# Performance work log

Measured on AMD Instinct MI355X. Metric: run time of the kernel, lower is better.

Reference implementation:

```python
import jax, jax.numpy as jnp
import numpy as np
from jax import lax

B, S, D, F, E, K = 4, 2048, 2048, 8192, 8, 2


def setup_inputs() -> dict:
    key = jax.random.key(0)
    ks = jax.random.split(key, 4)
    sd = 1.0 / np.sqrt(D)
    sf = 1.0 / np.sqrt(F)
    return {
        "hidden_states": jax.random.normal(ks[0], (B, S, D), dtype=jnp.float32),
        "router_w": jax.random.normal(ks[1], (D, E), dtype=jnp.float32) * sd,
        "w1": jax.random.normal(ks[2], (E, D, F), dtype=jnp.float32) * sd,
        "b1": jnp.zeros((E, F), dtype=jnp.float32),
        "w2": jax.random.normal(ks[3], (E, F, D), dtype=jnp.float32) * sf,
        "b2": jnp.zeros((E, D), dtype=jnp.float32),
        "top_k": K,
    }


def reference(hidden_states, router_w, w1, b1, w2, b2, top_k):
    b, s, d = hidden_states.shape
    x = hidden_states.reshape(-1, d)  # [T, D] flat tokens
    # Router: top-k over expert logits, softmax over the selected logits.
    logits = x @ router_w                      # [T, E]
    top_vals, top_idx = lax.top_k(logits, top_k)  # [T, K]
    scores = jax.nn.softmax(top_vals, axis=-1)    # [T, K]

    out = jnp.zeros_like(x)
    n_experts = w1.shape[0]
    for e in range(n_experts):  # fixed small expert count
        # per-token combine weight for this expert (0 if not routed)
        cw = jnp.sum(jnp.where(top_idx == e, scores, 0.0), axis=-1)  # [T]
        h = jax.nn.gelu(x @ w1[e] + b1[e], approximate=False)        # [T, F]
        out = out + cw[:, None] * (h @ w2[e] + b2[e])                # masked combine
    out = out.reshape(b, s, d)
    return out + hidden_states  # use_residual=True
```

## Files before the change

### kernel.cpp

```cpp
#include <hip/hip_runtime.h>

#define T_TOK 8192
#define DIM   2048
#define FFN   8192
#define NE    8
#define TOPK  2

typedef unsigned short ushort_t;
typedef unsigned short ushort8  __attribute__((ext_vector_type(8)));
typedef unsigned short ushort4v __attribute__((ext_vector_type(4)));
typedef short bf16x8 __attribute__((ext_vector_type(8)));
typedef float f32x4  __attribute__((ext_vector_type(4)));

__device__ __forceinline__ ushort_t f2bf(float f) {
  unsigned int u = __float_as_uint(f);
  u += 0x7FFFu + ((u >> 16) & 1u);
  return (ushort_t)(u >> 16);
}
__device__ __forceinline__ float bf2f(ushort_t u) {
  return __uint_as_float(((unsigned int)u) << 16);
}

__device__ __forceinline__ void gload16(const void* g, void* l) {
  __builtin_amdgcn_global_load_lds((const __attribute__((address_space(1))) void*)g,
                                   (__attribute__((address_space(3))) void*)l, 16, 0, 0);
}
__device__ __forceinline__ unsigned lds_off(const ushort_t* p) {
  return (unsigned)(uintptr_t)(__attribute__((address_space(3))) const ushort_t*)p;
}
__device__ __forceinline__ bf16x8 ds_read128(unsigned off) {
  bf16x8 r;
  asm volatile("ds_read_b128 %0, %1" : "=v"(r) : "v"(off));
  return r;
}

__device__ __forceinline__ float gelu_exact(float v) {
  float s = v * 0.70710678118654752f;
  float a = fabsf(s);
  float t = __builtin_amdgcn_rcpf(1.0f + 0.3275911f * a);
  float p = t * (0.254829592f +
            t * (-0.284496736f +
            t * (1.421413741f +
            t * (-1.453152027f +
            t * 1.061405429f))));
  float er = 1.0f - p * __expf(-a * a);
  er = copysignf(er, s);
  return 0.5f * v * (1.0f + er);
}

__global__ void k_cast(const float* __restrict__ x, ushort_t* __restrict__ xbf) {
  int i = blockIdx.x * blockDim.x + threadIdx.x;
  float4 v = reinterpret_cast<const float4*>(x)[i];
  ushort4v o;
  o.x = f2bf(v.x); o.y = f2bf(v.y); o.z = f2bf(v.z); o.w = f2bf(v.w);
  reinterpret_cast<ushort4v*>(xbf)[i] = o;
}

#define TT 64
__global__ __launch_bounds__(256) void k_wcvt(const float* __restrict__ in,
                                              ushort_t* __restrict__ outp, int R, int C) {
  __shared__ ushort_t t[TT][TT + 8];
  int e = blockIdx.z;
  const float* src = in + (size_t)e * R * C;
  ushort_t* dst = outp + (size_t)e * R * C;
  int r0 = blockIdx.y * TT, c0 = blockIdx.x * TT;
  int tid = threadIdx.x;
  int rr = tid >> 4;
  int c4 = tid & 15;
#pragma unroll
  for (int i = 0; i < 4; i++) {
    int r = rr + i * 16;
    float4 v = *reinterpret_cast<const float4*>(src + (size_t)(r0 + r) * C + c0 + c4 * 4);
    ushort4v p;
    p.x = f2bf(v.x); p.y = f2bf(v.y); p.z = f2bf(v.z); p.w = f2bf(v.w);
    *reinterpret_cast<ushort4v*>(&t[r][c4 * 4]) = p;
  }
  __syncthreads();
  int c = tid >> 2, rs = tid & 3;
  ushort_t tmp[16];
#pragma unroll
  for (int i = 0; i < 16; i++) tmp[i] = t[rs * 16 + i][c];
  ushort8 v0, v1;
#pragma unroll
  for (int i = 0; i < 8; i++) { v0[i] = tmp[i]; v1[i] = tmp[8 + i]; }
  ushort_t* drow = dst + (size_t)(c0 + c) * R + r0 + rs * 16;
  *reinterpret_cast<ushort8*>(drow) = v0;
  *reinterpret_cast<ushort8*>(drow + 8) = v1;
}

__global__ __launch_bounds__(256) void k_router(
    const float* __restrict__ x, const float* __restrict__ rw,
    int* __restrict__ tidx, float* __restrict__ twt, int* __restrict__ counts) {
  int t = blockIdx.x;
  int tid = threadIdx.x;
  int lane = tid & 63, wave = tid >> 6;
  float acc[NE];
#pragma unroll
  for (int e = 0; e < NE; e++) acc[e] = 0.f;
  const float* xr = x + (size_t)t * DIM;
  for (int d = tid; d < DIM; d += 256) {
    float xv = xr[d];
    const float* r = rw + d * NE;
#pragma unroll
    for (int e = 0; e < NE; e++) acc[e] += xv * r[e];
  }
  __shared__ float wsum[4][NE];
#pragma unroll
  for (int e = 0; e < NE; e++) {
    float v = acc[e];
#pragma unroll
    for (int off = 32; off > 0; off >>= 1) v += __shfl_down(v, off);
    if (lane == 0) wsum[wave][e] = v;
  }
  __syncthreads();
  if (tid == 0) {
    float lg[NE];
#pragma unroll
    for (int e = 0; e < NE; e++) lg[e] = wsum[0][e] + wsum[1][e] + wsum[2][e] + wsum[3][e];
    int i0 = 0; float v0 = lg[0];
#pragma unroll
    for (int e = 1; e < NE; e++) if (lg[e] > v0) { v0 = lg[e]; i0 = e; }
    int i1 = -1; float v1 = -3.4e38f;
#pragma unroll
    for (int e = 0; e < NE; e++) if (e != i0 && lg[e] > v1) { v1 = lg[e]; i1 = e; }
    float e1 = expf(v1 - v0);
    float s = 1.f + e1;
    tidx[t * 2 + 0] = i0; tidx[t * 2 + 1] = i1;
    twt[t * 2 + 0] = 1.f / s; twt[t * 2 + 1] = e1 / s;
    atomicAdd(&counts[i0], 1);
    atomicAdd(&counts[i1], 1);
  }
}

__global__ void k_scan(const int* __restrict__ counts, int* __restrict__ offsets) {
  if (threadIdx.x == 0) {
    int s = 0;
    for (int e = 0; e < NE; e++) { offsets[e] = s; s += counts[e]; }
    offsets[NE] = s;
  }
}

__global__ void k_fill(const int* __restrict__ tidx, const float* __restrict__ twt,
                       const int* __restrict__ offsets, int* __restrict__ cursors,
                       int* __restrict__ ltok, float* __restrict__ lwt, int* __restrict__ ppos) {
  int t = blockIdx.x * blockDim.x + threadIdx.x;
  if (t >= T_TOK) return;
#pragma unroll
  for (int k = 0; k < TOPK; k++) {
    int e = tidx[t * 2 + k];
    int pos = atomicAdd(&cursors[e], 1);
    int p = offsets[e] + pos;
    ltok[p] = t;
    lwt[p] = twt[t * 2 + k];
    ppos[t * 2 + k] = p;
  }
}

#define BM 256
#define BN 256
#define BK 32
#define SLOT (BM * BK)
#define SLOTB (SLOT * 2)

__device__ __forceinline__ void xcd_decode(int lin, int nwg, int nx, int& xt, int& yt) {
  int q = nwg >> 3;
  int w = (lin & 7) * q + (lin >> 3);
  xt = w % nx;
  yt = w / nx;
}

template <int NT>
__device__ __forceinline__ void gemm_loop(const ushort_t* __restrict__ a0,
                                          const ushort_t* __restrict__ a1,
                                          const ushort_t* __restrict__ b0,
                                          const ushort_t* __restrict__ b1,
                                          ushort_t* AsLds, ushort_t* BsLds,
                                          f32x4 (&acc)[8][4]) {
  int tid = threadIdx.x;
  int wid = tid >> 6, lane = tid & 63;
  int wm = wid >> 2, wn = wid & 3;
  int lm = lane & 15, lg = lane >> 4;

  unsigned abase = lds_off(AsLds), bbase = lds_off(BsLds);
  unsigned aoff[8], boff[4];
#pragma unroll
  for (int m = 0; m < 8; m++)
    aoff[m] = abase + (unsigned)(((wm * 128 + m * 16 + lm) * BK + lg * 8) * 2);
#pragma unroll
  for (int n = 0; n < 4; n++)
    boff[n] = bbase + (unsigned)(((wn * 64 + n * 16 + lm) * BK + lg * 8) * 2);

  const ushort_t* ap[2] = {a0, a1};
  const ushort_t* bp[2] = {b0, b1};

  auto STAGE = [&](int buf, int k0) {
#pragma unroll
    for (int j = 0; j < 2; j++) {
      gload16(ap[j] + k0, AsLds + buf * SLOT + (j * 512 + wid * 64) * 8);
      gload16(bp[j] + k0, BsLds + buf * SLOT + (j * 512 + wid * 64) * 8);
    }
  };

  STAGE(0, 0);
  STAGE(1, BK);
  int cur = 0;
  for (int t = 0; t < NT; ++t) {
    int s2 = cur + 2; if (s2 >= 3) s2 -= 3;
    if (t + 2 < NT) {
      STAGE(s2, (t + 2) * BK);
      __builtin_amdgcn_sched_barrier(0);
      asm volatile("s_waitcnt vmcnt(8)" ::: "memory");
    } else if (t + 1 < NT) {
      __builtin_amdgcn_sched_barrier(0);
      asm volatile("s_waitcnt vmcnt(4)" ::: "memory");
    } else {
      __builtin_amdgcn_sched_barrier(0);
      asm volatile("s_waitcnt vmcnt(0)" ::: "memory");
    }
    __builtin_amdgcn_s_barrier();
    __builtin_amdgcn_sched_barrier(0);
    unsigned cb = (unsigned)(cur * SLOTB);
    bf16x8 af[8], bv[4];
#pragma unroll
    for (int m = 0; m < 8; m++) af[m] = ds_read128(aoff[m] + cb);
#pragma unroll
    for (int n = 0; n < 4; n++) bv[n] = ds_read128(boff[n] + cb);
    asm volatile("s_waitcnt lgkmcnt(0)" ::: "memory");
    __builtin_amdgcn_sched_barrier(0);
    __builtin_amdgcn_s_setprio(1);
#pragma unroll
    for (int m = 0; m < 8; m++)
#pragma unroll
      for (int n = 0; n < 4; n++)
        acc[m][n] = __builtin_amdgcn_mfma_f32_16x16x32_bf16(af[m], bv[n], acc[m][n], 0, 0, 0);
    __builtin_amdgcn_s_setprio(0);
    __builtin_amdgcn_sched_barrier(0);
    __builtin_amdgcn_s_barrier();
    __builtin_amdgcn_sched_barrier(0);
    cur += 1; if (cur == 3) cur = 0;
  }
}

__global__ __launch_bounds__(512) void k_gemm1(
    const ushort_t* __restrict__ xbf, const ushort_t* __restrict__ w1t, const float* __restrict__ b1,
    const int* __restrict__ counts, const int* __restrict__ offsets,
    const int* __restrict__ ltok, ushort_t* __restrict__ H) {
  int e = blockIdx.z;
  int cnt = counts[e];
  int xt, yt;
  xcd_decode(blockIdx.x, (T_TOK / BM) * (FFN / BN), T_TOK / BM, xt, yt);
  int row0 = xt * BM;
  if (row0 >= cnt) return;
  int base = offsets[e];
  int col0 = yt * BN;
  const ushort_t* Bt = w1t + (size_t)e * DIM * FFN;

  __shared__ __align__(16) ushort_t As[3 * SLOT];
  __shared__ __align__(16) ushort_t Bs[3 * SLOT];

  int tid = threadIdx.x;
  int rsub = tid >> 2, seg = tid & 3;
  const ushort_t* asrc[2]; const ushort_t* bsrc[2];
#pragma unroll
  for (int j = 0; j < 2; j++) {
    int row = j * 128 + rsub;
    int ar = min(row0 + row, cnt - 1);
    asrc[j] = xbf + (size_t)ltok[base + ar] * DIM + seg * 8;
    bsrc[j] = Bt + (size_t)(col0 + row) * DIM + seg * 8;
  }
  f32x4 acc[8][4];
#pragma unroll
  for (int m = 0; m < 8; m++)
#pragma unroll
    for (int n = 0; n < 4; n++) acc[m][n] = (f32x4){0.f, 0.f, 0.f, 0.f};

  gemm_loop<DIM / BK>(asrc[0], asrc[1], bsrc[0], bsrc[1], As, Bs, acc);

  int wid = tid >> 6, lane = tid & 63;
  int wm = wid >> 2, wn = wid & 3;
  int lm = lane & 15, lg = lane >> 4;
#pragma unroll
  for (int m = 0; m < 8; m++) {
#pragma unroll
    for (int n = 0; n < 4; n++) {
      int f = col0 + wn * 64 + n * 16 + lm;
      float bias = b1[e * FFN + f];
#pragma unroll
      for (int r = 0; r < 4; r++) {
        int row = row0 + wm * 128 + m * 16 + lg * 4 + r;
        if (row < cnt) {
          float v = acc[m][n][r] + bias;
          H[(size_t)(base + row) * FFN + f] = f2bf(gelu_exact(v));
        }
      }
    }
  }
}

__global__ __launch_bounds__(512) void k_gemm2(
    const ushort_t* __restrict__ H, const ushort_t* __restrict__ w2t, const float* __restrict__ b2,
    const int* __restrict__ counts, const int* __restrict__ offsets,
    const float* __restrict__ lwt, ushort_t* __restrict__ contrib) {
  int e = blockIdx.z;
  int cnt = counts[e];
  int xt, yt;
  xcd_decode(blockIdx.x, (T_TOK / BM) * (DIM / BN), T_TOK / BM, xt, yt);
  int row0 = xt * BM;
  if (row0 >= cnt) return;
  int base = offsets[e];
  int col0 = yt * BN;
  const ushort_t* Bt = w2t + (size_t)e * DIM * FFN;

  __shared__ __align__(16) ushort_t As[3 * SLOT];
  __shared__ __align__(16) ushort_t Bs[3 * SLOT];

  int tid = threadIdx.x;
  int rsub = tid >> 2, seg = tid & 3;
  const ushort_t* asrc[2]; const ushort_t* bsrc[2];
#pragma unroll
  for (int j = 0; j < 2; j++) {
    int row = j * 128 + rsub;
    int ar = min(row0 + row, cnt - 1);
    asrc[j] = H + (size_t)(base + ar) * FFN + seg * 8;
    bsrc[j] = Bt + (size_t)(col0 + row) * FFN + seg * 8;
  }
  f32x4 acc[8][4];
#pragma unroll
  for (int m = 0; m < 8; m++)
#pragma unroll
    for (int n = 0; n < 4; n++) acc[m][n] = (f32x4){0.f, 0.f, 0.f, 0.f};

  gemm_loop<FFN / BK>(asrc[0], asrc[1], bsrc[0], bsrc[1], As, Bs, acc);

  int wid = tid >> 6, lane = tid & 63;
  int wm = wid >> 2, wn = wid & 3;
  int lm = lane & 15, lg = lane >> 4;
#pragma unroll
  for (int m = 0; m < 8; m++) {
#pragma unroll
    for (int n = 0; n < 4; n++) {
      int d = col0 + wn * 64 + n * 16 + lm;
      float bias = b2[e * DIM + d];
#pragma unroll
      for (int r = 0; r < 4; r++) {
        int row = row0 + wm * 128 + m * 16 + lg * 4 + r;
        if (row < cnt) {
          float v = (acc[m][n][r] + bias) * lwt[base + row];
          contrib[(size_t)(base + row) * DIM + d] = f2bf(v);
        }
      }
    }
  }
}

__global__ void k_combine(const float* __restrict__ x, const ushort_t* __restrict__ contrib,
                          const int* __restrict__ ppos, float* __restrict__ out) {
  int i = blockIdx.x * blockDim.x + threadIdx.x;
  int t = i / (DIM / 4);
  int dq = i % (DIM / 4);
  int p0 = ppos[t * 2 + 0], p1 = ppos[t * 2 + 1];
  float4 xv = reinterpret_cast<const float4*>(x)[i];
  ushort4v c0 = reinterpret_cast<const ushort4v*>(contrib + (size_t)p0 * DIM)[dq];
  ushort4v c1 = reinterpret_cast<const ushort4v*>(contrib + (size_t)p1 * DIM)[dq];
  float4 o;
  o.x = xv.x + bf2f(c0.x) + bf2f(c1.x);
  o.y = xv.y + bf2f(c0.y) + bf2f(c1.y);
  o.z = xv.z + bf2f(c0.z) + bf2f(c1.z);
  o.w = xv.w + bf2f(c0.w) + bf2f(c1.w);
  reinterpret_cast<float4*>(out)[i] = o;
}

extern "C" void kernel_launch(void* const* d_in, const int* in_sizes, int n_in,
                              void* d_out, int out_size, void* d_ws, size_t ws_size,
                              hipStream_t stream) {
  const float* x  = (const float*)d_in[0];
  const float* rw = (const float*)d_in[1];
  const float* w1 = (const float*)d_in[2];
  const float* b1 = (const float*)d_in[3];
  const float* w2 = (const float*)d_in[4];
  const float* b2 = (const float*)d_in[5];
  float* out = (float*)d_out;
  char* ws = (char*)d_ws;

  const size_t MB = 1u << 20;
  int*   counts  = (int*)(ws);
  int*   offsets = (int*)(ws + 64);
  int*   cursors = (int*)(ws + 128);
  int*   tidx    = (int*)(ws + 1 * MB);
  float* twt     = (float*)(ws + 2 * MB);
  int*   ltok    = (int*)(ws + 3 * MB);
  float* lwt     = (float*)(ws + 4 * MB);
  int*   ppos    = (int*)(ws + 5 * MB);
  ushort_t* xbf     = (ushort_t*)(ws + 8 * MB);
  ushort_t* contrib = (ushort_t*)(ws + 8 * MB);
  ushort_t* Hbuf    = (ushort_t*)(ws + 72 * MB);
  ushort_t* w1t     = (ushort_t*)(ws + 328 * MB);
  ushort_t* w2t     = (ushort_t*)(ws + 328 * MB);
  const size_t NEED = 584 * MB;
  if (ws_size < NEED) {
    hipMemsetAsync(d_out, 0, (size_t)out_size * sizeof(float), stream);
    return;
  }

  hipMemsetAsync(ws, 0, 256, stream);
  k_cast<<<dim3((T_TOK * (size_t)DIM / 4) / 256), 256, 0, stream>>>(x, xbf);
  k_router<<<T_TOK, 256, 0, stream>>>(x, rw, tidx, twt, counts);
  k_scan<<<1, 64, 0, stream>>>(counts, offsets);
  k_fill<<<T_TOK / 256, 256, 0, stream>>>(tidx, twt, offsets, cursors, ltok, lwt, ppos);
  k_wcvt<<<dim3(FFN / TT, DIM / TT, NE), 256, 0, stream>>>(w1, w1t, DIM, FFN);
  k_gemm1<<<dim3((T_TOK / BM) * (FFN / BN), 1, NE), 512, 0, stream>>>(xbf, w1t, b1, counts, offsets, ltok, Hbuf);
  k_wcvt<<<dim3(DIM / TT, FFN / TT, NE), 256, 0, stream>>>(w2, w2t, FFN, DIM);
  k_gemm2<<<dim3((T_TOK / BM) * (DIM / BN), 1, NE), 512, 0, stream>>>(Hbuf, w2t, b2, counts, offsets, lwt, contrib);
  k_combine<<<dim3((T_TOK * (size_t)DIM / 4) / 256), 256, 0, stream>>>(x, contrib, ppos, out);
}
```

Before: 2.338 ms.

## XOR-swizzle LDS tiles and interleave A-fragment reads with MFMA groups

Applies an XOR swizzle to the 16-byte chunk position within each LDS row, on both the global-to-LDS staging side and the ds_read side. The aim is to cut LDS bank conflicts on the 128-bit reads. It also splits the per-tile MFMA block into four groups, reading two A fragments per group so LDS reads overlap with the previous group's MFMAs and fewer fragment registers are live. The extra s_barrier inside each group adds workgroup-wide synchronisation that could stall warps.

```diff
diff --git a/kernel.cpp b/kernel.cpp
--- a/kernel.cpp
+++ b/kernel.cpp
@@ -180,15 +180,16 @@
   int wid = tid >> 6, lane = tid & 63;
   int wm = wid >> 2, wn = wid & 3;
   int lm = lane & 15, lg = lane >> 4;
+  int pc = lg ^ (lm & 3);
 
   unsigned abase = lds_off(AsLds), bbase = lds_off(BsLds);
   unsigned aoff[8], boff[4];
 #pragma unroll
   for (int m = 0; m < 8; m++)
-    aoff[m] = abase + (unsigned)(((wm * 128 + m * 16 + lm) * BK + lg * 8) * 2);
+    aoff[m] = abase + (unsigned)(((wm * 128 + m * 16 + lm) * BK + pc * 8) * 2);
 #pragma unroll
   for (int n = 0; n < 4; n++)
-    boff[n] = bbase + (unsigned)(((wn * 64 + n * 16 + lm) * BK + lg * 8) * 2);
+    boff[n] = bbase + (unsigned)(((wn * 64 + n * 16 + lm) * BK + pc * 8) * 2);
 
   const ushort_t* ap[2] = {a0, a1};
   const ushort_t* bp[2] = {b0, b1};
@@ -220,20 +221,37 @@
     __builtin_amdgcn_s_barrier();
     __builtin_amdgcn_sched_barrier(0);
     unsigned cb = (unsigned)(cur * SLOTB);
-    bf16x8 af[8], bv[4];
-#pragma unroll
-    for (int m = 0; m < 8; m++) af[m] = ds_read128(aoff[m] + cb);
+
+    bf16x8 bv[4], af0, af1;
 #pragma unroll
     for (int n = 0; n < 4; n++) bv[n] = ds_read128(boff[n] + cb);
+    af0 = ds_read128(aoff[0] + cb);
+    af1 = ds_read128(aoff[1] + cb);
     asm volatile("s_waitcnt lgkmcnt(0)" ::: "memory");
     __builtin_amdgcn_sched_barrier(0);
     __builtin_amdgcn_s_setprio(1);
 #pragma unroll
-    for (int m = 0; m < 8; m++)
-#pragma unroll
-      for (int n = 0; n < 4; n++)
-        acc[m][n] = __builtin_amdgcn_mfma_f32_16x16x32_bf16(af[m], bv[n], acc[m][n], 0, 0, 0);
+    for (int n = 0; n < 4; n++) {
+      acc[0][n] = __builtin_amdgcn_mfma_f32_16x16x32_bf16(af0, bv[n], acc[0][n], 0, 0, 0);
+      acc[1][n] = __builtin_amdgcn_mfma_f32_16x16x32_bf16(af1, bv[n], acc[1][n], 0, 0, 0);
+    }
     __builtin_amdgcn_s_setprio(0);
+#pragma unroll
+    for (int q = 1; q < 4; q++) {
+      bf16x8 nf0 = ds_read128(aoff[2 * q] + cb);
+      bf16x8 nf1 = ds_read128(aoff[2 * q + 1] + cb);
+      __builtin_amdgcn_sched_barrier(0);
+      __builtin_amdgcn_s_barrier();
+      asm volatile("s_waitcnt lgkmcnt(0)" ::: "memory");
+      __builtin_amdgcn_sched_barrier(0);
+      __builtin_amdgcn_s_setprio(1);
+#pragma unroll
+      for (int n = 0; n < 4; n++) {
+        acc[2 * q][n]     = __builtin_amdgcn_mfma_f32_16x16x32_bf16(nf0, bv[n], acc[2 * q][n], 0, 0, 0);
+        acc[2 * q + 1][n] = __builtin_amdgcn_mfma_f32_16x16x32_bf16(nf1, bv[n], acc[2 * q + 1][n], 0, 0, 0);
+      }
+      __builtin_amdgcn_s_setprio(0);
+    }
     __builtin_amdgcn_sched_barrier(0);
     __builtin_amdgcn_s_barrier();
     __builtin_amdgcn_sched_barrier(0);
@@ -259,7 +277,8 @@
   __shared__ __align__(16) ushort_t Bs[3 * SLOT];
 
   int tid = threadIdx.x;
-  int rsub = tid >> 2, seg = tid & 3;
+  int rsub = tid >> 2;
+  int seg = (tid & 3) ^ (rsub & 3);
   const ushort_t* asrc[2]; const ushort_t* bsrc[2];
 #pragma unroll
   for (int j = 0; j < 2; j++) {
@@ -315,7 +334,8 @@
   __shared__ __align__(16) ushort_t Bs[3 * SLOT];
 
   int tid = threadIdx.x;
-  int rsub = tid >> 2, seg = tid & 3;
+  int rsub = tid >> 2;
+  int seg = (tid & 3) ^ (rsub & 3);
   const ushort_t* asrc[2]; const ushort_t* bsrc[2];
 #pragma unroll
   for (int j = 0; j < 2; j++) {
```

After: 2.322 ms. No clear change (-0.7%).
